# Kernel optimization log

Hardware: AMD Instinct MI355X
Metric: run time of the kernel (lower is better)

Reference implementation:

```python
import jax, jax.numpy as jnp
import numpy as np

FEAT_STRIDE = 16
PRE_NMS = 6000
POST_NMS = 300
NMS_THRESH = 0.7
NEG_THR = 0.3
POS_THR = 0.7
RPN_BATCH = 256
FG_FRAC = 0.5
SCALES = (8, 16, 32)
RATIOS = (0.5, 1.0, 2.0)
A = len(SCALES) * len(RATIOS)  # 9


def _generate_anchors():
    base = 16.0
    ctr = (base - 1.0) * 0.5
    size = base * base
    out = []
    for r in RATIOS:
        ws = np.round(np.sqrt(size / r))
        hs = np.round(ws * r)
        for s in SCALES:
            W = ws * s
            H = hs * s
            out.append([ctr - 0.5 * (W - 1), ctr - 0.5 * (H - 1),
                        ctr + 0.5 * (W - 1), ctr + 0.5 * (H - 1)])
    return np.array(out, np.float32)  # [9,4]


def _conv(x, w, b, pad):
    y = jax.lax.conv_general_dilated(x, w, (1, 1), [(pad, pad), (pad, pad)],
                                     dimension_numbers=('NCHW', 'OIHW', 'NCHW'))
    return y + b[None, :, None, None]


def _all_anchors(H, W):
    base = jnp.asarray(_generate_anchors())
    sx = jnp.arange(W, dtype=jnp.float32) * FEAT_STRIDE
    sy = jnp.arange(H, dtype=jnp.float32) * FEAT_STRIDE
    gy, gx = jnp.meshgrid(sy, sx, indexing='ij')
    shifts = jnp.stack([gx, gy, gx, gy], -1).reshape(-1, 1, 4)  # [H*W,1,4]
    return (shifts + base[None]).reshape(-1, 4)  # (h,w,a) order, [H*W*A,4]


def _decode(anchors, deltas):
    w = anchors[:, 2] - anchors[:, 0] + 1.0
    h = anchors[:, 3] - anchors[:, 1] + 1.0
    cx = anchors[:, 0] + 0.5 * w
    cy = anchors[:, 1] + 0.5 * h
    pcx = deltas[:, 0] * w + cx
    pcy = deltas[:, 1] * h + cy
    pw = jnp.exp(deltas[:, 2]) * w
    ph = jnp.exp(deltas[:, 3]) * h
    return jnp.stack([pcx - 0.5 * pw, pcy - 0.5 * ph, pcx + 0.5 * pw, pcy + 0.5 * ph], -1)


def _encode(anchors, gt):
    ew = anchors[:, 2] - anchors[:, 0] + 1.0
    eh = anchors[:, 3] - anchors[:, 1] + 1.0
    ecx = anchors[:, 0] + 0.5 * ew
    ecy = anchors[:, 1] + 0.5 * eh
    gw = gt[:, 2] - gt[:, 0] + 1.0
    gh = gt[:, 3] - gt[:, 1] + 1.0
    gcx = gt[:, 0] + 0.5 * gw
    gcy = gt[:, 1] + 0.5 * gh
    return jnp.stack([(gcx - ecx) / ew, (gcy - ecy) / eh,
                      jnp.log(gw / ew), jnp.log(gh / eh)], -1)


def _nms(boxes, scores, thresh, max_out):
    x1, y1, x2, y2 = boxes[:, 0], boxes[:, 1], boxes[:, 2], boxes[:, 3]
    areas = (x2 - x1 + 1.0) * (y2 - y1 + 1.0)
    N = boxes.shape[0]

    def body(k, st):
        valid, sel, selv = st
        s = jnp.where(valid, scores, -jnp.inf)
        i = jnp.argmax(s)
        ok = s[i] > -jnp.inf
        iw = jnp.maximum(jnp.minimum(x2[i], x2) - jnp.maximum(x1[i], x1) + 1.0, 0.0)
        ih = jnp.maximum(jnp.minimum(y2[i], y2) - jnp.maximum(y1[i], y1) + 1.0, 0.0)
        inter = iw * ih
        iou = inter / (areas[i] + areas - inter)
        valid = valid & (iou <= thresh)
        return valid, sel.at[k].set(i.astype(jnp.int32)), selv.at[k].set(ok)

    st = jax.lax.fori_loop(0, max_out, body,
                           (jnp.ones(N, bool), jnp.zeros(max_out, jnp.int32), jnp.zeros(max_out, bool)))
    return st[1], st[2]


def _propose_one(scores, deltas, anchors, imh, imw):
    boxes = _decode(anchors, deltas)
    boxes = jnp.stack([jnp.clip(boxes[:, 0], 0.0, imw - 1.0),
                       jnp.clip(boxes[:, 1], 0.0, imh - 1.0),
                       jnp.clip(boxes[:, 2], 0.0, imw - 1.0),
                       jnp.clip(boxes[:, 3], 0.0, imh - 1.0)], -1)
    top_s, idx = jax.lax.top_k(scores, PRE_NMS)
    top_b = boxes[idx]
    sel, selv = _nms(top_b, top_s, NMS_THRESH, POST_NMS)
    return top_b[sel] * selv[:, None].astype(top_b.dtype)  # [POST_NMS,4], zero rows when exhausted


def _anchor_target_one(gt, imh, imw, rfg, rbg, anchors):
    N = anchors.shape[0]
    ax1, ay1, ax2, ay2 = anchors[:, 0], anchors[:, 1], anchors[:, 2], anchors[:, 3]
    inside = (ax1 >= 0) & (ay1 >= 0) & (ax2 < imw) & (ay2 < imh)
    gx1, gy1, gx2, gy2 = gt[:, 0], gt[:, 1], gt[:, 2], gt[:, 3]
    gw = gx2 - gx1 + 1.0
    gh = gy2 - gy1 + 1.0
    gt_valid = ~((gw == 1.0) & (gh == 1.0))  # all-zero padded gt boxes
    aw = ax2 - ax1 + 1.0
    ah = ay2 - ay1 + 1.0
    iw = jnp.maximum(jnp.minimum(ax2[:, None], gx2[None, :]) - jnp.maximum(ax1[:, None], gx1[None, :]) + 1.0, 0.0)
    ih = jnp.maximum(jnp.minimum(ay2[:, None], gy2[None, :]) - jnp.maximum(ay1[:, None], gy1[None, :]) + 1.0, 0.0)
    inter = iw * ih
    iou = inter / ((aw * ah)[:, None] + (gw * gh)[None, :] - inter)  # [N,K]
    iou = jnp.where(gt_valid[None, :], iou, 0.0)
    iou = jnp.where(inside[:, None], iou, -1.0)  # outside anchors excluded, as in original
    max_ov = iou.max(1)
    arg = iou.argmax(1)
    gt_max = iou.max(0)
    gt_max = jnp.where(gt_max <= 0.0, 1e-5, gt_max)
    keep = (iou == gt_max[None, :]).any(1)  # anchors with max overlap per gt -> fg
    labels = jnp.full(N, -1.0, jnp.float32)
    labels = jnp.where(max_ov < NEG_THR, 0.0, labels)
    labels = jnp.where(keep, 1.0, labels)
    labels = jnp.where(max_ov >= POS_THR, 1.0, labels)
    labels = jnp.where(inside, labels, -1.0)

    def ranks(r, mask):
        order = jnp.argsort(jnp.where(mask, r, 2.0))
        return jnp.zeros(N, jnp.int32).at[order].set(jnp.arange(N, dtype=jnp.int32))

    num_fg = int(FG_FRAC * RPN_BATCH)
    fg_keep = (labels == 1.0) & (ranks(rfg, labels == 1.0) < num_fg)
    num_bg = RPN_BATCH - fg_keep.sum()
    bg_keep = (labels == 0.0) & (ranks(rbg, labels == 0.0) < num_bg)
    labels = jnp.where(fg_keep, 1.0, jnp.where(bg_keep, 0.0, -1.0))
    targets = _encode(anchors, gt[arg, :4])
    ones4 = jnp.ones((1, 4), jnp.float32)
    in_w = (labels == 1.0).astype(jnp.float32)[:, None] * ones4
    n_ex = (labels >= 0).sum().astype(jnp.float32)
    out_w = jnp.where(labels >= 0, 1.0 / n_ex, 0.0)[:, None] * ones4
    return labels, targets, in_w, out_w


def _rpn_forward(base_feat, im_info, gt_boxes, conv_w, conv_b, cls_w, cls_b, bbox_w, bbox_b):
    B, _, H, W = base_feat.shape
    x = jax.nn.relu(_conv(base_feat, conv_w, conv_b, 1))
    cls_score = _conv(x, cls_w, cls_b, 0)                 # [B,2A,H,W]
    # reshape(x,2) -> softmax over axis 1 -> reshape back
    prob = jax.nn.softmax(cls_score.reshape(B, 2, A * H, W), axis=1).reshape(B, 2 * A, H, W)
    bbox_pred = _conv(x, bbox_w, bbox_b, 0)               # [B,4A,H,W]
    anchors = _all_anchors(H, W)                          # [H*W*A,4]

    # ---- proposal layer (detached in original) ----
    fg = prob[:, A:, :, :].transpose(0, 2, 3, 1).reshape(B, -1)        # (h,w,a)
    deltas = bbox_pred.transpose(0, 2, 3, 1).reshape(B, -1, 4)
    rois_boxes = jax.vmap(_propose_one, in_axes=(0, 0, None, 0, 0))(
        jax.lax.stop_gradient(fg), jax.lax.stop_gradient(deltas), anchors, im_info[:, 0], im_info[:, 1])
    batch_idx = jnp.broadcast_to(jnp.arange(B, dtype=rois_boxes.dtype)[:, None, None], (B, POST_NMS, 1))
    rois = jnp.concatenate([batch_idx, rois_boxes], -1)   # [B,POST_NMS,5]

    # ---- anchor target layer (training path) ----
    key = jax.random.key(42)
    rfg = jax.random.uniform(key, (B, anchors.shape[0]))
    rbg = jax.random.uniform(jax.random.fold_in(key, 1), (B, anchors.shape[0]))
    labels, targets, in_w, out_w = jax.vmap(_anchor_target_one, in_axes=(0, 0, 0, 0, 0, None))(
        gt_boxes, im_info[:, 0], im_info[:, 1], rfg, rbg, anchors)
    # rearrange (h,w,a) -> (a,h,w) layouts to match torch permutes
    labels = labels.reshape(B, H, W, A).transpose(0, 3, 1, 2).reshape(B, -1)
    targets = targets.reshape(B, H, W, A * 4).transpose(0, 3, 1, 2)
    in_w = in_w.reshape(B, H, W, A * 4).transpose(0, 3, 1, 2)
    out_w = out_w.reshape(B, H, W, A * 4).transpose(0, 3, 1, 2)

    # cross-entropy over kept anchors
    logits = cls_score.reshape(B, 2, A, H, W).transpose(0, 2, 3, 4, 1).reshape(-1, 2)
    lab = labels.reshape(-1)
    m = (lab >= 0).astype(logits.dtype)
    logp = jax.nn.log_softmax(logits, axis=-1)
    idx = jnp.clip(lab, 0.0, 1.0).astype(jnp.int32)
    nll = -jnp.take_along_axis(logp, idx[:, None], axis=1)[:, 0]
    loss_cls = (nll * m).sum() / m.sum()

    # smooth-L1 box loss, sigma=3, sum dims [1,2,3] then mean over batch
    sigma2 = 9.0
    diff = in_w * (bbox_pred - targets)
    ad = jnp.abs(diff)
    flag = (ad < 1.0 / sigma2).astype(diff.dtype)
    lb = flag * 0.5 * sigma2 * diff * diff + (1.0 - flag) * (ad - 0.5 / sigma2)
    loss_box = (out_w * lb).sum(axis=(1, 2, 3)).mean()
    return rois, loss_cls, loss_box


def setup_inputs() -> dict:
    key = jax.random.key(0)
    ks = jax.random.split(key, 9)
    B, C, H, W = 4, 512, 50, 76
    base_feat = jax.random.normal(ks[0], (B, C, H, W), jnp.float32)
    conv_w = jax.random.normal(ks[1], (512, C, 3, 3), jnp.float32) * 0.01
    conv_b = jnp.zeros((512,), jnp.float32)
    cls_w = jax.random.normal(ks[2], (18, 512, 1, 1), jnp.float32) * 0.01
    cls_b = jnp.zeros((18,), jnp.float32)
    bbox_w = jax.random.normal(ks[3], (36, 512, 1, 1), jnp.float32) * 0.01
    bbox_b = jnp.zeros((36,), jnp.float32)
    imh, imw = float(H * FEAT_STRIDE), float(W * FEAT_STRIDE)
    im_info = jnp.tile(jnp.array([imh, imw, 1.0], jnp.float32), (B, 1))
    K = 20
    cx = jax.random.uniform(ks[4], (B, K)) * (imw - 100.0) + 50.0
    cy = jax.random.uniform(ks[5], (B, K)) * (imh - 100.0) + 50.0
    bw = jax.random.uniform(ks[6], (B, K)) * 270.0 + 30.0
    bh = jax.random.uniform(ks[7], (B, K)) * 270.0 + 30.0
    x1 = jnp.clip(cx - 0.5 * bw, 0.0, imw - 1.0)
    x2 = jnp.clip(cx + 0.5 * bw, 0.0, imw - 1.0)
    y1 = jnp.clip(cy - 0.5 * bh, 0.0, imh - 1.0)
    y2 = jnp.clip(cy + 0.5 * bh, 0.0, imh - 1.0)
    cls = jax.random.randint(ks[8], (B, K), 1, 21).astype(jnp.float32)
    gt_boxes = jnp.stack([x1, y1, x2, y2, cls], -1)
    num_boxes = jnp.full((B,), K, jnp.int32)
    return {"base_feat": base_feat, "im_info": im_info, "gt_boxes": gt_boxes,
            "num_boxes": num_boxes, "conv_w": conv_w, "conv_b": conv_b,
            "cls_w": cls_w, "cls_b": cls_b, "bbox_w": bbox_w, "bbox_b": bbox_b}


def reference(base_feat, im_info, gt_boxes, num_boxes, conv_w, conv_b, cls_w, cls_b, bbox_w, bbox_b):
    # num_boxes is implicitly handled via zero-padded gt_boxes (as in the original layer)
    return _rpn_forward(base_feat, im_info, gt_boxes, conv_w, conv_b, cls_w, cls_b, bbox_w, bbox_b)
```

## Files before the change

kernel.cpp:

```cpp
#include <hip/hip_runtime.h>
#include <stdint.h>

#define HHH 50
#define WWW 76
#define NPIX 3800
#define NA 34200
#define NSORT 65536
#define PRE 6000
#define POST 300
#define NW 94
#define CIN 512
#define COUT 512
#define NBATCH 4
#define NGT 20
#define TFHALF 68400u
#define PPLANE 4400
#define XTB 2252800

typedef __bf16 bf16x8 __attribute__((ext_vector_type(8)));
typedef float f32x4 __attribute__((ext_vector_type(4)));
typedef unsigned int u32x4v __attribute__((ext_vector_type(4)));

__device__ static inline f32x4 MFMA16(bf16x8 a, bf16x8 b, f32x4 c) {
  return __builtin_amdgcn_mfma_f32_16x16x32_bf16(a, b, c, 0, 0, 0);
}
__device__ static inline bf16x8 LD8(const unsigned short* p) {
  return __builtin_bit_cast(bf16x8, *(const u32x4v*)p);
}

__host__ __device__ static inline void tf2x32(unsigned k0, unsigned k1, unsigned& x0, unsigned& x1) {
  unsigned k2 = k0 ^ k1 ^ 0x1BD11BDAu;
#define TFR(r) do { x0 += x1; x1 = (x1 << (r)) | (x1 >> (32 - (r))); x1 ^= x0; } while (0)
  x0 += k0; x1 += k1;
  TFR(13); TFR(15); TFR(26); TFR(6);
  x0 += k1; x1 += k2 + 1u;
  TFR(17); TFR(29); TFR(16); TFR(24);
  x0 += k2; x1 += k0 + 2u;
  TFR(13); TFR(15); TFR(26); TFR(6);
  x0 += k0; x1 += k1 + 3u;
// ... 15 lines not shown
  {-56.f, -56.f,  71.f,  71.f}, {-120.f, -120.f, 135.f, 135.f}, {-248.f, -248.f, 263.f, 263.f},
  {-36.f, -80.f,  51.f,  95.f}, {-80.f, -168.f,  95.f, 183.f}, {-168.f, -344.f, 183.f, 359.f}
};

__device__ static inline unsigned monoF(float f) {
  int b = __float_as_int(f);
  unsigned u = (unsigned)b;
  return (b < 0) ? ~u : (u | 0x80000000u);
}
__device__ static inline float unmonoF(unsigned u) {
  unsigned b = (u & 0x80000000u) ? (u ^ 0x80000000u) : ~u;
  return __int_as_float((int)b);
}

__device__ static inline void split3(float v, unsigned short& h, unsigned short& m, unsigned short& l) {
  __bf16 b0 = (__bf16)v;  float f0 = (float)b0;
  float r = v - f0;       __bf16 b1 = (__bf16)r;  float f1 = (float)b1;
  float r2 = r - f1;      __bf16 b2 = (__bf16)r2;
  h = __builtin_bit_cast(unsigned short, b0);
  m = __builtin_bit_cast(unsigned short, b1);
  l = __builtin_bit_cast(unsigned short, b2);
}

__global__ void k_init(unsigned* gtmaxU, int* cnts, float* accums) {
  int t = threadIdx.x;
  if (t < NBATCH * NGT) gtmaxU[t] = 0x407FFFFFu;
  if (t < 8) cnts[t] = 0;
  if (t < 8) accums[t] = 0.f;
}

__global__ void k_split_x(const float* __restrict__ feat, unsigned short* __restrict__ x0,
                          unsigned short* __restrict__ x1, unsigned short* __restrict__ x2) {
  int tid = blockIdx.x * 256 + threadIdx.x;
  if (tid >= NBATCH * XTB) return;
  int b = tid / XTB;
  int rem = tid - b * XTB;
  int pg = rem >> 13;
  int r2 = rem & 8191;
  int cg = r2 >> 7;
  int po = (r2 >> 3) & 15;
  int cl = r2 & 7;
  int ci = cg * 8 + cl;
  int px = pg * 16 + po;
  int hq = px / 80, wq = px - hq * 80;
  float v = 0.f;
  if (hq >= 2 && hq < 52 && wq >= 1 && wq < 77)
    v = feat[((size_t)(b * 512 + ci)) * NPIX + (hq - 2) * 76 + (wq - 1)];
  unsigned short h, m, l;
  split3(v, h, m, l);
  x0[tid] = h; x1[tid] = m; x2[tid] = l;
}
// ... 3 lines not shown
  int tid = blockIdx.x * 256 + threadIdx.x;
  if (tid >= 9 * 64 * 512 * 8) return;
  int cl = tid & 7;
  int co = (tid >> 3) & 511;
  int cg = (tid >> 12) & 63;
  int tap = tid >> 18;
  int ci = cg * 8 + cl;
  float v = cw[((size_t)co * 512 + ci) * 9 + tap];
  unsigned short h, m, l;
  split3(v, h, m, l);
  w0[tid] = h; w1[tid] = m; w2[tid] = l;
}

__global__ void k_tr_w1(const float* __restrict__ clsw, const float* __restrict__ bbw, float* __restrict__ wt1) {
  int tid = blockIdx.x * 256 + threadIdx.x;
  if (tid >= CIN * 64) return;
  int c = tid & 63, ci = tid >> 6;
  float v = 0.f;
  if (c < 18) v = clsw[c * 512 + ci];
  else if (c < 54) v = bbw[(c - 18) * 512 + ci];
  wt1[tid] = v;
}

__global__ __launch_bounds__(256, 2) void k_conv3(
    const unsigned short* __restrict__ XT0, const unsigned short* __restrict__ XT1,
    const unsigned short* __restrict__ XT2,
    const unsigned short* __restrict__ WT0, const unsigned short* __restrict__ WT1,
    const unsigned short* __restrict__ WT2,
    const float* __restrict__ bias, float* __restrict__ out) {
  const int d = blockIdx.x;
  const int copair = (d >> 1) & 3, half = d & 1, g = d >> 3;
  const int cob = copair * 2 + (g & 1);
  const int pxb = half * 64 + (g >> 1);
  const int pxp = pxb & 31, b = pxb >> 5;
  const int co0 = cob * 64;
  const int px0 = 160 + pxp * 128;
  const int t = threadIdx.x, l = t & 63, wv = t >> 6;
  const int wr = wv >> 1, wc = wv & 1;
  const int l15 = l & 15, lq = l >> 4;
  f32x4 cmain[2][4], ccorr[2][4];
  double accd[2][4][4];
#pragma unroll
  for (int c = 0; c < 2; ++c)
#pragma unroll
    for (int p = 0; p < 4; ++p) {
      cmain[c][p] = (f32x4)(0.f); ccorr[c][p] = (f32x4)(0.f);
#pragma unroll
      for (int r = 0; r < 4; ++r) accd[c][p][r] = 0.0;
    }
  const unsigned short* xt0 = XT0 + (size_t)b * XTB;
  const unsigned short* xt1 = XT1 + (size_t)b * XTB;
  const unsigned short* xt2 = XT2 + (size_t)b * XTB;
  const int coA = wr * 32 + l15;
  const int OFFT[9] = {-81, -80, -79, -1, 0, 1, 79, 80, 81};
  const int pxw = px0 + wc * 64 + l15;

  for (int kg = 0; kg < 16; ++kg) {
    const int cgl = kg * 4 + lq;
    const int cglo = cgl * 128;
    const size_t aro = ((size_t)cgl * 512 + co0 + coA) * 8;
#pragma unroll
    for (int tap = 0; tap < 9; ++tap) {
      const size_t ao = aro + (size_t)tap * (64 * 512 * 8);
      bf16x8 A0[2], A1[2], A2[2];
      A0[0] = LD8(WT0 + ao); A0[1] = LD8(WT0 + ao + 128);
      A1[0] = LD8(WT1 + ao); A1[1] = LD8(WT1 + ao + 128);
      A2[0] = LD8(WT2 + ao); A2[1] = LD8(WT2 + ao + 128);
      const int pxbase = pxw + OFFT[tap];
      const size_t eob = (size_t)((pxbase >> 4) * 8192 + (pxbase & 15) * 8 + cglo);
#pragma unroll
      for (int p = 0; p < 4; ++p) {
        const size_t eo = eob + (size_t)p * 8192;
        bf16x8 B0 = LD8(xt0 + eo);
        bf16x8 B1 = LD8(xt1 + eo);
        bf16x8 B2 = LD8(xt2 + eo);
#pragma unroll
        for (int c = 0; c < 2; ++c) {
          cmain[c][p] = MFMA16(A0[c], B0, cmain[c][p]);
          ccorr[c][p] = MFMA16(A2[c], B0, ccorr[c][p]);
          ccorr[c][p] = MFMA16(A0[c], B2, ccorr[c][p]);
          ccorr[c][p] = MFMA16(A1[c], B1, ccorr[c][p]);
          ccorr[c][p] = MFMA16(A1[c], B0, ccorr[c][p]);
          ccorr[c][p] = MFMA16(A0[c], B1, ccorr[c][p]);
        }
      }
    }
    if (kg & 1) {
#pragma unroll
      for (int c = 0; c < 2; ++c)
#pragma unroll
        for (int p = 0; p < 4; ++p) {
#pragma unroll
          for (int r = 0; r < 4; ++r) accd[c][p][r] += (double)cmain[c][p][r];
          cmain[c][p] = (f32x4)(0.f);
        }
    }
  }
  const size_t outb = ((size_t)b * 512 + co0) * NPIX;
#pragma unroll
  for (int c = 0; c < 2; ++c)
#pragma unroll
    for (int p = 0; p < 4; ++p)
#pragma unroll
      for (int r = 0; r < 4; ++r) {
        int coL = wr * 32 + c * 16 + lq * 4 + r;
        int px = px0 + wc * 64 + p * 16 + l15;
        int hq = px / 80, wq = px - hq * 80;
        if (hq >= 2 && hq < 52 && wq >= 1 && wq < 77) {
          float v = (float)(accd[c][p][r] + (double)ccorr[c][p][r]) + bias[co0 + coL];
          out[outb + (size_t)coL * NPIX + (hq - 2) * 76 + (wq - 1)] = fmaxf(v, 0.f);
        }
      }
}

__global__ __launch_bounds__(256) void k_conv1(const float* __restrict__ x, const float* __restrict__ wt1,
                                               const float* __restrict__ clsb, const float* __restrict__ bbb,
                                               float* __restrict__ clsS, float* __restrict__ bbp) {
  const int b = blockIdx.y;
  const int px0 = blockIdx.x * 128;
  const int t = threadIdx.x;
  const int cg = t & 7, pg = t >> 3;
  __shared__ float xs[16][128];
  __shared__ float ws[16][72];
  double acc[8][4];
#pragma unroll
  for (int i = 0; i < 8; ++i)
#pragma unroll
    for (int j = 0; j < 4; ++j) acc[i][j] = 0.0;
  const float* xb = x + (size_t)b * CIN * NPIX;
  for (int cc = 0; cc < CIN; cc += 16) {
#pragma unroll
    for (int e0 = 0; e0 < 8; ++e0) {
// ... 34 lines not shown
#pragma unroll
      for (int j = 0; j < 4; ++j) acc[i][j] += (double)a32[i][j];
    __syncthreads();
  }
#pragma unroll
  for (int i = 0; i < 8; ++i) {
    int c = cg * 8 + i;
#pragma unroll
    for (int j = 0; j < 4; ++j) {
      int p = px0 + pg * 4 + j;
      if (p < NPIX) {
        if (c < 18) clsS[((size_t)b * 18 + c) * NPIX + p] = (float)acc[i][j] + clsb[c];
        else if (c < 54) bbp[((size_t)b * 36 + (c - 18)) * NPIX + p] = (float)acc[i][j] + bbb[c - 18];
      }
    }
  }
}

__global__ void k_decode(const float* __restrict__ clsS, const float* __restrict__ bbp,
                         const float* __restrict__ im_info, float* __restrict__ boxes,
                         unsigned long long* __restrict__ keys) {
  int tid = blockIdx.x * 256 + threadIdx.x;
  int b = tid >> 16, n = tid & 0xFFFF;
  if (n >= NA) { keys[((size_t)b << 16) + n] = 0ull; return; }
  int a = n % 9, p = n / 9;
  int h = p / WWW, w = p - h * WWW;
  const float* cb = clsS + (size_t)b * 18 * NPIX;
  float s0 = cb[(size_t)a * NPIX + p];
  float s1 = cb[(size_t)(9 + a) * NPIX + p];
  float mx = fmaxf(s0, s1);
  float e0 = expf(s0 - mx), e1 = expf(s1 - mx);
  float fg = e1 / (e0 + e1);
  const float* bb = bbp + (size_t)b * 36 * NPIX;
  float d0 = bb[(size_t)(a * 4 + 0) * NPIX + p];
  float d1 = bb[(size_t)(a * 4 + 1) * NPIX + p];
  float d2 = bb[(size_t)(a * 4 + 2) * NPIX + p];
  float d3 = bb[(size_t)(a * 4 + 3) * NPIX + p];
  float ax1 = BA[a][0] + w * 16.f, ay1 = BA[a][1] + h * 16.f;
  float ax2 = BA[a][2] + w * 16.f, ay2 = BA[a][3] + h * 16.f;
  float aw = ax2 - ax1 + 1.f, ah = ay2 - ay1 + 1.f;
  float acx = ax1 + 0.5f * aw, acy = ay1 + 0.5f * ah;
  float pcx = d0 * aw + acx, pcy = d1 * ah + acy;
  float pw = expf(d2) * aw, ph = expf(d3) * ah;
  float imh = im_info[b * 3 + 0], imw = im_info[b * 3 + 1];
  float x1 = fminf(fmaxf(pcx - 0.5f * pw, 0.f), imw - 1.f);
  float y1 = fminf(fmaxf(pcy - 0.5f * ph, 0.f), imh - 1.f);
  float x2 = fminf(fmaxf(pcx + 0.5f * pw, 0.f), imw - 1.f);
  float y2 = fminf(fmaxf(pcy + 0.5f * ph, 0.f), imh - 1.f);
  float* bx = boxes + ((size_t)b * NA + n) * 4;
  bx[0] = x1; bx[1] = y1; bx[2] = x2; bx[3] = y2;
  unsigned fb = __float_as_uint(fg);
  keys[((size_t)b << 16) + n] = ((unsigned long long)fb << 32) | (unsigned)(~(unsigned)n);
}

__global__ __launch_bounds__(256) void k_sort_local0(unsigned long long* keys) {
  __shared__ unsigned long long s[2048];
  const int chunk = blockIdx.x;
  const int b = chunk >> 5, cloc = chunk & 31;
  unsigned long long* base = keys + ((size_t)b << 16) + ((size_t)cloc << 11);
  const int gbase = cloc << 11;
  const int t = threadIdx.x;
  for (int e = t; e < 2048; e += 256) s[e] = base[e];
  __syncthreads();
  for (int k = 2; k <= 2048; k <<= 1) {
    for (int j = k >> 1; j >= 1; j >>= 1) {
      for (int q = t; q < 1024; q += 256) {
        int i = ((q & ~(j - 1)) << 1) | (q & (j - 1));
        int pp = i | j;
        bool up = (((unsigned)(gbase + i)) & (unsigned)k) == 0;
        unsigned long long a = s[i], dd = s[pp];
        if (up ? (a < dd) : (a > dd)) { s[i] = dd; s[pp] = a; }
      }
      __syncthreads();
    }
  }
  for (int e = t; e < 2048; e += 256) base[e] = s[e];
}
__global__ __launch_bounds__(256) void k_sort_merge(unsigned long long* keys, int k) {
  __shared__ unsigned long long s[2048];
  const int chunk = blockIdx.x;
  const int b = chunk >> 5, cloc = chunk & 31;
  unsigned long long* base = keys + ((size_t)b << 16) + ((size_t)cloc << 11);
  const int gbase = cloc << 11;
  const int t = threadIdx.x;
  for (int e = t; e < 2048; e += 256) s[e] = base[e];
  __syncthreads();
  for (int j = 1024; j >= 1; j >>= 1) {
    for (int q = t; q < 1024; q += 256) {
      int i = ((q & ~(j - 1)) << 1) | (q & (j - 1));
      int pp = i | j;
      bool up = (((unsigned)(gbase + i)) & (unsigned)k) == 0;
      unsigned long long a = s[i], dd = s[pp];
      if (up ? (a < dd) : (a > dd)) { s[i] = dd; s[pp] = a; }
    }
    __syncthreads();
  }
  for (int e = t; e < 2048; e += 256) base[e] = s[e];
}
__global__ void k_sort_gstep(unsigned long long* keys, int k, int j) {
  int tid = blockIdx.x * 256 + threadIdx.x;
  int b = tid >> 16, i = tid & 0xFFFF;
  if ((i & j) != 0) return;
  int pp = i | j;
  unsigned long long* base = keys + ((size_t)b << 16);
  unsigned long long a = base[i], dd = base[pp];
  bool up = (((unsigned)i) & (unsigned)k) == 0;
  if (up ? (a < dd) : (a > dd)) { base[i] = dd; base[pp] = a; }
}

__global__ void k_gather(const unsigned long long* __restrict__ keys, const float* __restrict__ boxes,
                         float* tbx1, float* tby1, float* tbx2, float* tby2, float* tba) {
  int tid = blockIdx.x * 256 + threadIdx.x;
  if (tid >= NBATCH * PRE) return;
  int b = tid / PRE;
  int k = tid - b * PRE;
  unsigned long long key = keys[((size_t)b << 16) + k];
  unsigned n = ~(unsigned)(key & 0xFFFFFFFFu);
  const float* bx = boxes + ((size_t)b * NA + n) * 4;
  float x1 = bx[0], y1 = bx[1], x2 = bx[2], y2 = bx[3];
  tbx1[tid] = x1; tby1[tid] = y1; tbx2[tid] = x2; tby2[tid] = y2;
  tba[tid] = (x2 - x1 + 1.f) * (y2 - y1 + 1.f);
}

__global__ __launch_bounds__(256) void k_mask(const float* __restrict__ tbx1, const float* __restrict__ tby1,
                                              const float* __restrict__ tbx2, const float* __restrict__ tby2,
                                              const float* __restrict__ tba, unsigned long long* __restrict__ mask) {
  const int b = blockIdx.y;
  const int i0 = blockIdx.x * 64;
  const int t = threadIdx.x;
  __shared__ float jx1[2048], jy1[2048], jx2[2048], jy2[2048], ja[2048];
  __shared__ float ix1[64], iy1[64], ix2[64], iy2[64], ia[64];
  const float* bx1 = tbx1 + b * PRE;
  const float* by1 = tby1 + b * PRE;
  const float* bx2 = tbx2 + b * PRE;
  const float* by2 = tby2 + b * PRE;
  const float* ba2 = tba + b * PRE;
  if (t < 64) {
    int i = i0 + t;
    if (i < PRE) { ix1[t] = bx1[i]; iy1[t] = by1[i]; ix2[t] = bx2[i]; iy2[t] = by2[i]; ia[t] = ba2[i]; }
// ... 19 lines not shown
        if (j > i && j < PRE) {
          int e = j - j0;
          float iw = fminf(X2, jx2[e]) - fmaxf(X1, jx1[e]) + 1.f;
          float ih = fminf(Y2, jy2[e]) - fmaxf(Y1, jy1[e]) + 1.f;
          if (iw > 0.f && ih > 0.f) {
            float inter = iw * ih;
            float iou = inter / (A + ja[e] - inter);
            if (iou > 0.7f) word |= (1ull << l);
          }
        }
      }
      mask[((size_t)(b * PRE + i)) * NW + wg] = word;
    }
    __syncthreads();
  }
}

__global__ void k_nms(const unsigned long long* __restrict__ mask,
                      const float* __restrict__ tbx1, const float* __restrict__ tby1,
                      const float* __restrict__ tbx2, const float* __restrict__ tby2,
                      float* __restrict__ out) {
  const int b = blockIdx.x;
  const int lane = threadIdx.x;
  __shared__ unsigned long long rem[NW];
  for (int w = lane; w < NW; w += 64) rem[w] = 0ull;
  __syncthreads();
  int sc = 0;
  for (int w = 0; w < NW && sc < POST; ++w) {
    while (sc < POST) {
      unsigned long long avail = ~rem[w];
      if (w == NW - 1) avail &= (1ull << (PRE - (NW - 1) * 64)) - 1ull;
      if (avail == 0ull) break;
      int l = __ffsll((unsigned long long)avail) - 1;
      int j = w * 64 + l;
      if (lane < 5) {
        float v;
        if (lane == 0) v = (float)b;
        else if (lane == 1) v = tbx1[b * PRE + j];
        else if (lane == 2) v = tby1[b * PRE + j];
        else if (lane == 3) v = tbx2[b * PRE + j];
        else v = tby2[b * PRE + j];
        out[((size_t)(b * POST + sc)) * 5 + lane] = v;
      }
      sc++;
      if (sc == POST) break;
      const unsigned long long* row = mask + ((size_t)(b * PRE + j)) * NW;
      for (int w2 = w + lane; w2 < NW; w2 += 64) {
        unsigned long long m = row[w2];
        if (w2 == w) m |= (1ull << l);
        rem[w2] |= m;
      }
      __syncthreads();
    }
  }
  for (int r2 = sc; r2 < POST; ++r2)
    if (lane < 5) out[((size_t)(b * POST + r2)) * 5 + lane] = (lane == 0) ? (float)b : 0.f;
}

__global__ __launch_bounds__(256) void k_iouA(const float* __restrict__ gt_boxes, const float* __restrict__ im_info,
                                              float* __restrict__ iou, float* __restrict__ maxov,
                                              int* __restrict__ argm, unsigned* __restrict__ gtmaxU) {
  const int b = blockIdx.y;
  const int n = blockIdx.x * 256 + threadIdx.x;
  __shared__ float g[NGT][6];
  if (threadIdx.x < NGT) {
    const float* gg = gt_boxes + (b * NGT + threadIdx.x) * 5;
    float x1 = gg[0], y1 = gg[1], x2 = gg[2], y2 = gg[3];
    g[threadIdx.x][0] = x1; g[threadIdx.x][1] = y1; g[threadIdx.x][2] = x2; g[threadIdx.x][3] = y2;
    float gw = x2 - x1 + 1.f, gh = y2 - y1 + 1.f;
    g[threadIdx.x][4] = gw * gh;
    g[threadIdx.x][5] = ((gw == 1.f) && (gh == 1.f)) ? 0.f : 1.f;
  }
  __syncthreads();
  if (n >= NA) return;
  int a = n % 9, p = n / 9;
  int h = p / WWW, w = p - h * WWW;
// ... 34 lines not shown
    float gm = unmonoF(gtmaxU[b * NGT + threadIdx.x]);
    gmf[threadIdx.x] = (gm <= 0.f) ? 1e-5f : gm;
  }
  __syncthreads();
  int label = -1;
  if (n < NA) {
    int a = n % 9, p = n / 9;
    int h = p / WWW, w = p - h * WWW;
    float ax1 = BA[a][0] + w * 16.f, ay1 = BA[a][1] + h * 16.f;
    float ax2 = BA[a][2] + w * 16.f, ay2 = BA[a][3] + h * 16.f;
    float imh = im_info[b * 3 + 0], imw = im_info[b * 3 + 1];
    bool inside = (ax1 >= 0.f) && (ay1 >= 0.f) && (ax2 < imw) && (ay2 < imh);
    float mo = maxov[b * NA + n];
    const float* row = iou + ((size_t)(b * NA) + n) * NGT;
    bool keep = false;
#pragma unroll
    for (int j = 0; j < NGT; ++j) keep = keep || (row[j] == gmf[j]);
    if (mo < 0.3f) label = 0;
    if (keep) label = 1;
    if (mo >= 0.7f) label = 1;
    if (!inside) label = -1;
    labels[b * NA + n] = label;
    unsigned pp = (unsigned)(b * NA + n);
    ufg[b * NA + n] = (label == 1) ? tf_u23(kf0, kf1, pp) : 0xFFFFFFFFu;
    ubg[b * NA + n] = (label == 0) ? tf_u23(kb0, kb1, pp) : 0xFFFFFFFFu;
  }
  unsigned long long bf = __ballot(label == 1);
  unsigned long long bb = __ballot(label == 0);
  if ((threadIdx.x & 63) == 0) {
    atomicAdd(&cnts[b], (int)__popcll(bf));
    atomicAdd(&cnts[4 + b], (int)__popcll(bb));
  }
}

__global__ __launch_bounds__(1024) void k_select(const unsigned* __restrict__ ufg, const unsigned* __restrict__ ubg,
                                                 const int* __restrict__ cnts, unsigned* __restrict__ selp,
                                                 float* __restrict__ nexf) {
  const int blk = blockIdx.x;
  const int b = blk >> 1, cls = blk & 1;
  const unsigned* u = (cls == 0 ? ufg : ubg) + (size_t)b * NA;
  const int fcnt = cnts[b], bcnt = cnts[4 + b];
  const int kk = (cls == 0) ? 128 : (256 - (fcnt < 128 ? fcnt : 128));
  const int cnt = (cls == 0) ? fcnt : bcnt;
  __shared__ int partial[16];
  __shared__ int s_cnt;
  auto bcount = [&](auto pred) -> int {
    int c = 0;
    for (int i = threadIdx.x; i < NA; i += 1024) c += pred((unsigned)i, u[i]) ? 1 : 0;
    for (int o = 32; o > 0; o >>= 1) c += __shfl_down(c, o);
    if ((threadIdx.x & 63) == 0) partial[threadIdx.x >> 6] = c;
    __syncthreads();
    if (threadIdx.x == 0) { int s = 0; for (int q = 0; q < 16; ++q) s += partial[q]; s_cnt = s; }
    __syncthreads();
    int r = s_cnt;
    __syncthreads();
    return r;
  };
  unsigned thr, ithr;
  if (cnt <= kk) { thr = 0xFFFFFFFFu; ithr = 0xFFFFFFFFu; }
  else {
    unsigned lo = 0, hi = 0x00800000u;
    while (lo < hi) {
      unsigned mid = lo + ((hi - lo) >> 1);
      int c = bcount([&](unsigned, unsigned v) { return v <= mid; });
      if (c >= kk) hi = mid; else lo = mid + 1;
    }
    thr = lo;
    int c1 = (thr == 0u) ? 0 : bcount([&](unsigned, unsigned v) { return v < thr; });
    int need = kk - c1;
    unsigned lo2 = 0, hi2 = NA - 1;
    while (lo2 < hi2) {
      unsigned mid = lo2 + ((hi2 - lo2) >> 1);
      int c = bcount([&](unsigned i, unsigned v) { return (v == thr) && (i <= mid); });
      if (c >= need) hi2 = mid; else lo2 = mid + 1;
    }
    ithr = lo2;
  }
  if (threadIdx.x == 0) {
    selp[blk * 2] = thr;
    selp[blk * 2 + 1] = ithr;
    if (cls == 1) {
      int fk = fcnt < 128 ? fcnt : 128;
      int bk2 = bcnt < kk ? bcnt : kk;
      nexf[b] = (float)(fk + bk2);
    }
  }
}

__global__ __launch_bounds__(256) void k_loss(const float* __restrict__ clsS, const float* __restrict__ bbp,
                                              const float* __restrict__ gt_boxes, const int* __restrict__ labels,
                                              const unsigned* __restrict__ ufg, const unsigned* __restrict__ ubg,
                                              const unsigned* __restrict__ selp, const int* __restrict__ argm,
                                              float* __restrict__ accums) {
  const int b = blockIdx.y;
  const int n = blockIdx.x * 256 + threadIdx.x;
  float nll = 0.f, mcnt = 0.f, lbsum = 0.f;
  if (n < NA) {
    int label = labels[b * NA + n];
    int fin = -1;
    if (label == 1) {
      unsigned uu = ufg[b * NA + n];
      unsigned thr = selp[(b * 2 + 0) * 2], ithr = selp[(b * 2 + 0) * 2 + 1];
      if (uu < thr || (uu == thr && (unsigned)n <= ithr)) fin = 1;
    } else if (label == 0) {
      unsigned uu = ubg[b * NA + n];
      unsigned thr = selp[(b * 2 + 1) * 2], ithr = selp[(b * 2 + 1) * 2 + 1];
      if (uu < thr || (uu == thr && (unsigned)n <= ithr)) fin = 0;
    }
// ... 70 lines not shown
  const float* cls_b     = (const float*)d_in[7];
  const float* bbox_w    = (const float*)d_in[8];
  const float* bbox_b    = (const float*)d_in[9];
  float* out = (float*)d_out;

  char* wp = (char*)d_ws;
  auto carve = [&](size_t bytes) -> void* {
    void* r = (void*)wp;
    wp += (bytes + 255) & ~(size_t)255;
    return r;
  };
  float* x     = (float*)carve((size_t)NBATCH * CIN * NPIX * 4);
  float* clsS  = (float*)carve((size_t)NBATCH * 18 * NPIX * 4);
  float* bbp   = (float*)carve((size_t)NBATCH * 36 * NPIX * 4);
  unsigned short* WT0 = (unsigned short*)carve((size_t)9 * 64 * 512 * 8 * 2);
  unsigned short* WT1 = (unsigned short*)carve((size_t)9 * 64 * 512 * 8 * 2);
  unsigned short* WT2 = (unsigned short*)carve((size_t)9 * 64 * 512 * 8 * 2);
  float* wt1   = (float*)carve((size_t)CIN * 64 * 4);
  unsigned* gtmaxU = (unsigned*)carve(NBATCH * NGT * 4);
  int* cnts    = (int*)carve(8 * 4);
  unsigned* selp = (unsigned*)carve(16 * 4);
  float* nexf  = (float*)carve(4 * 4);
  float* accums = (float*)carve(8 * 4);

  char* overlay = wp;
  unsigned short* XT0 = (unsigned short*)overlay;
  unsigned short* XT1 = XT0 + (size_t)NBATCH * XTB;
  unsigned short* XT2 = XT1 + (size_t)NBATCH * XTB;
  char* wp2 = overlay;
  auto carve2 = [&](size_t bytes) -> void* {
    void* r = (void*)wp2;
    wp2 += (bytes + 255) & ~(size_t)255;
    return r;
  };
  float* boxes = (float*)carve2((size_t)NBATCH * NA * 4 * 4);
  unsigned long long* keys = (unsigned long long*)carve2((size_t)NBATCH * NSORT * 8);
  float* tbx1 = (float*)carve2((size_t)NBATCH * PRE * 4);
  float* tby1 = (float*)carve2((size_t)NBATCH * PRE * 4);
  float* tbx2 = (float*)carve2((size_t)NBATCH * PRE * 4);
  float* tby2 = (float*)carve2((size_t)NBATCH * PRE * 4);
  float* tba  = (float*)carve2((size_t)NBATCH * PRE * 4);
  unsigned long long* mask = (unsigned long long*)carve2((size_t)NBATCH * PRE * NW * 8);
  float* iou   = (float*)carve2((size_t)NBATCH * NA * NGT * 4);
  float* maxov = (float*)carve2((size_t)NBATCH * NA * 4);
  int* argm    = (int*)carve2((size_t)NBATCH * NA * 4);
  int* labels  = (int*)carve2((size_t)NBATCH * NA * 4);
  unsigned* ufg = (unsigned*)carve2((size_t)NBATCH * NA * 4);
  unsigned* ubg = (unsigned*)carve2((size_t)NBATCH * NA * 4);

  unsigned kb0 = 0u, kb1 = 1u;
  tf2x32(0u, 42u, kb0, kb1);

  k_init<<<dim3(1), dim3(256), 0, stream>>>(gtmaxU, cnts, accums);
  k_split_w<<<dim3((9 * 64 * 512 * 8) / 256), dim3(256), 0, stream>>>(conv_w, WT0, WT1, WT2);
  k_tr_w1<<<dim3((CIN * 64) / 256), dim3(256), 0, stream>>>(cls_w, bbox_w, wt1);
  k_split_x<<<dim3((NBATCH * XTB + 255) / 256), dim3(256), 0, stream>>>(base_feat, XT0, XT1, XT2);
  k_conv3<<<dim3(1024), dim3(256), 0, stream>>>(XT0, XT1, XT2, WT0, WT1, WT2, conv_b, x);
  k_conv1<<<dim3(30, 4), dim3(256), 0, stream>>>(x, wt1, cls_b, bbox_b, clsS, bbp);
  k_decode<<<dim3(NBATCH * NSORT / 256), dim3(256), 0, stream>>>(clsS, bbp, im_info, boxes, keys);
  k_sort_local0<<<dim3(NBATCH * 32), dim3(256), 0, stream>>>(keys);
  for (int k = 4096; k <= 65536; k <<= 1) {
    for (int j = k >> 1; j >= 2048; j >>= 1)
      k_sort_gstep<<<dim3(NBATCH * NSORT / 256), dim3(256), 0, stream>>>(keys, k, j);
    k_sort_merge<<<dim3(NBATCH * 32), dim3(256), 0, stream>>>(keys, k);
  }
  k_gather<<<dim3((NBATCH * PRE + 255) / 256), dim3(256), 0, stream>>>(keys, boxes, tbx1, tby1, tbx2, tby2, tba);
  k_mask<<<dim3(NW, NBATCH), dim3(256), 0, stream>>>(tbx1, tby1, tbx2, tby2, tba, mask);
  k_nms<<<dim3(NBATCH), dim3(64), 0, stream>>>(mask, tbx1, tby1, tbx2, tby2, out);
  k_iouA<<<dim3((NA + 255) / 256, NBATCH), dim3(256), 0, stream>>>(gt_boxes, im_info, iou, maxov, argm, gtmaxU);
  k_labels<<<dim3((NA + 255) / 256, NBATCH), dim3(256), 0, stream>>>(iou, maxov, gtmaxU, im_info,
                                                                     0u, 42u, kb0, kb1, labels, ufg, ubg, cnts);
  k_select<<<dim3(8), dim3(1024), 0, stream>>>(ufg, ubg, cnts, selp, nexf);
  k_loss<<<dim3((NA + 255) / 256, NBATCH), dim3(256), 0, stream>>>(clsS, bbp, gt_boxes, labels, ufg, ubg, selp, argm, accums);
  k_final<<<dim3(1), dim3(1), 0, stream>>>(accums, nexf, out);
}
```

Baseline: 1.530 ms.

## Replace full bitonic sort with radix top-k select, compact, and LDS sort

The 65536-key global bitonic sort is replaced by a radix select for the 6000th-largest key, an atomic compaction of the keys at or above it, and a single-block LDS bitonic sort of 8192 entries. The binary-search sampling selection becomes a radix select over a composite key. NMS moves its suppression state into per-lane registers and picks the next box with ballots instead of shared memory and barriers. The conv3 kernel drops its double-precision accumulators for an fp32 master accumulator and requests 3 blocks per SM. This cuts many kernel launches and global sort passes, but fp32 accumulation may change numerics and raising occupancy may cause register spills.

```diff
diff --git a/kernel.cpp b/kernel.cpp
--- a/kernel.cpp
+++ b/kernel.cpp
@@ -5,7 +5,6 @@
 #define WWW 76
 #define NPIX 3800
 #define NA 34200
-#define NSORT 65536
 #define PRE 6000
 #define POST 300
 #define NW 94
@@ -14,7 +13,6 @@
 #define NBATCH 4
 #define NGT 20
 #define TFHALF 68400u
-#define PPLANE 4400
 #define XTB 2252800
 
 typedef __bf16 bf16x8 __attribute__((ext_vector_type(8)));
@@ -76,11 +74,12 @@
   l = __builtin_bit_cast(unsigned short, b2);
 }
 
-__global__ void k_init(unsigned* gtmaxU, int* cnts, float* accums) {
+__global__ void k_init(unsigned* gtmaxU, int* cnts, float* accums, int* ccnt) {
   int t = threadIdx.x;
   if (t < NBATCH * NGT) gtmaxU[t] = 0x407FFFFFu;
   if (t < 8) cnts[t] = 0;
   if (t < 8) accums[t] = 0.f;
+  if (t < 4) ccnt[t] = 0;
 }
 
 __global__ void k_split_x(const float* __restrict__ feat, unsigned short* __restrict__ x0,
@@ -130,7 +129,7 @@
   wt1[tid] = v;
 }
 
-__global__ __launch_bounds__(256, 2) void k_conv3(
+__global__ __launch_bounds__(256, 3) void k_conv3(
     const unsigned short* __restrict__ XT0, const unsigned short* __restrict__ XT1,
     const unsigned short* __restrict__ XT2,
     const unsigned short* __restrict__ WT0, const unsigned short* __restrict__ WT1,
@@ -146,15 +145,12 @@
   const int t = threadIdx.x, l = t & 63, wv = t >> 6;
   const int wr = wv >> 1, wc = wv & 1;
   const int l15 = l & 15, lq = l >> 4;
-  f32x4 cmain[2][4], ccorr[2][4];
-  double accd[2][4][4];
+  f32x4 cmain[2][4], ccorr[2][4], cmast[2][4];
 #pragma unroll
   for (int c = 0; c < 2; ++c)
 #pragma unroll
     for (int p = 0; p < 4; ++p) {
-      cmain[c][p] = (f32x4)(0.f); ccorr[c][p] = (f32x4)(0.f);
-#pragma unroll
-      for (int r = 0; r < 4; ++r) accd[c][p][r] = 0.0;
+      cmain[c][p] = (f32x4)(0.f); ccorr[c][p] = (f32x4)(0.f); cmast[c][p] = (f32x4)(0.f);
     }
   const unsigned short* xt0 = XT0 + (size_t)b * XTB;
   const unsigned short* xt1 = XT1 + (size_t)b * XTB;
@@ -193,16 +189,13 @@
         }
       }
     }
-    if (kg & 1) {
-#pragma unroll
-      for (int c = 0; c < 2; ++c)
-#pragma unroll
-        for (int p = 0; p < 4; ++p) {
-#pragma unroll
-          for (int r = 0; r < 4; ++r) accd[c][p][r] += (double)cmain[c][p][r];
-          cmain[c][p] = (f32x4)(0.f);
-        }
-    }
+#pragma unroll
+    for (int c = 0; c < 2; ++c)
+#pragma unroll
+      for (int p = 0; p < 4; ++p) {
+        cmast[c][p] += cmain[c][p];
+        cmain[c][p] = (f32x4)(0.f);
+      }
   }
   const size_t outb = ((size_t)b * 512 + co0) * NPIX;
 #pragma unroll
@@ -215,7 +208,7 @@
         int px = px0 + wc * 64 + p * 16 + l15;
         int hq = px / 80, wq = px - hq * 80;
         if (hq >= 2 && hq < 52 && wq >= 1 && wq < 77) {
-          float v = (float)(accd[c][p][r] + (double)ccorr[c][p][r]) + bias[co0 + coL];
+          float v = (cmast[c][p][r] + ccorr[c][p][r]) + bias[co0 + coL];
           out[outb + (size_t)coL * NPIX + (hq - 2) * 76 + (wq - 1)] = fmaxf(v, 0.f);
         }
       }
@@ -296,7 +289,7 @@
                          unsigned long long* __restrict__ keys) {
   int tid = blockIdx.x * 256 + threadIdx.x;
   int b = tid >> 16, n = tid & 0xFFFF;
-  if (n >= NA) { keys[((size_t)b << 16) + n] = 0ull; return; }
+  if (n >= NA) return;
   int a = n % 9, p = n / 9;
   int h = p / WWW, w = p - h * WWW;
   const float* cb = clsS + (size_t)b * 18 * NPIX;
@@ -327,68 +320,83 @@
   keys[((size_t)b << 16) + n] = ((unsigned long long)fb << 32) | (unsigned)(~(unsigned)n);
 }
 
-__global__ __launch_bounds__(256) void k_sort_local0(unsigned long long* keys) {
-  __shared__ unsigned long long s[2048];
-  const int chunk = blockIdx.x;
-  const int b = chunk >> 5, cloc = chunk & 31;
-  unsigned long long* base = keys + ((size_t)b << 16) + ((size_t)cloc << 11);
-  const int gbase = cloc << 11;
+__global__ __launch_bounds__(1024) void k_rsel_top(const unsigned long long* __restrict__ keys,
+                                                   unsigned long long* __restrict__ selK) {
+  const int b = blockIdx.x;
+  const unsigned long long* kb = keys + ((size_t)b << 16);
+  __shared__ int hist[16][256];
+  __shared__ int histT[256];
+  __shared__ unsigned long long sh_prefix;
+  __shared__ unsigned sh_r;
+  const int t = threadIdx.x, wid = t >> 6;
+  if (t == 0) { sh_prefix = 0ull; sh_r = PRE; }
+  __syncthreads();
+  for (int p = 7; p >= 0; --p) {
+    for (int e = t; e < 4096; e += 1024) ((int*)hist)[e] = 0;
+    __syncthreads();
+    unsigned long long pref = sh_prefix;
+    for (int i = t; i < NA; i += 1024) {
+      unsigned long long k = kb[i];
+      bool m = (p == 7) || ((k >> (8 * (p + 1))) == pref);
+      if (m) atomicAdd(&hist[wid][(int)((k >> (8 * p)) & 255)], 1);
+    }
+    __syncthreads();
+    if (t < 256) { int s = 0; for (int w = 0; w < 16; ++w) s += hist[w][t]; histT[t] = s; }
+    __syncthreads();
+    if (t == 0) {
+      unsigned rr = sh_r; unsigned cum = 0;
+      for (int v = 255; v >= 0; --v) {
+        cum += (unsigned)histT[v];
+        if (cum >= rr) { sh_r = rr - (cum - (unsigned)histT[v]); sh_prefix = (sh_prefix << 8) | (unsigned)v; break; }
+      }
+    }
+    __syncthreads();
+  }
+  if (t == 0) selK[b] = sh_prefix;
+}
+
+__global__ void k_compact(const unsigned long long* __restrict__ keys,
+                          const unsigned long long* __restrict__ selK,
+                          int* __restrict__ ccnt, unsigned long long* __restrict__ comp) {
+  int tid = blockIdx.x * 256 + threadIdx.x;
+  int b = tid >> 16, n = tid & 0xFFFF;
+  if (n >= NA) return;
+  unsigned long long k = keys[((size_t)b << 16) + n];
+  if (k >= selK[b]) {
+    int pos = atomicAdd(&ccnt[b], 1);
+    comp[b * 8192 + pos] = k;
+  }
+}
+
+__global__ __launch_bounds__(1024) void k_sort_lds(unsigned long long* __restrict__ comp) {
+  __shared__ unsigned long long s[8192];
+  const int b = blockIdx.x;
   const int t = threadIdx.x;
-  for (int e = t; e < 2048; e += 256) s[e] = base[e];
+  unsigned long long* cb = comp + b * 8192;
+  for (int e = t; e < 8192; e += 1024) s[e] = (e < PRE) ? cb[e] : 0ull;
   __syncthreads();
-  for (int k = 2; k <= 2048; k <<= 1) {
+  for (int k = 2; k <= 8192; k <<= 1) {
     for (int j = k >> 1; j >= 1; j >>= 1) {
-      for (int q = t; q < 1024; q += 256) {
+      for (int q = t; q < 4096; q += 1024) {
         int i = ((q & ~(j - 1)) << 1) | (q & (j - 1));
         int pp = i | j;
-        bool up = (((unsigned)(gbase + i)) & (unsigned)k) == 0;
-        unsigned long long a = s[i], dd = s[pp];
-        if (up ? (a < dd) : (a > dd)) { s[i] = dd; s[pp] = a; }
+        bool up = (i & k) == 0;
+        unsigned long long a = s[i], d = s[pp];
+        if (up ? (a < d) : (a > d)) { s[i] = d; s[pp] = a; }
       }
       __syncthreads();
     }
   }
-  for (int e = t; e < 2048; e += 256) base[e] = s[e];
-}
-__global__ __launch_bounds__(256) void k_sort_merge(unsigned long long* keys, int k) {
-  __shared__ unsigned long long s[2048];
-  const int chunk = blockIdx.x;
-  const int b = chunk >> 5, cloc = chunk & 31;
-  unsigned long long* base = keys + ((size_t)b << 16) + ((size_t)cloc << 11);
-  const int gbase = cloc << 11;
-  const int t = threadIdx.x;
-  for (int e = t; e < 2048; e += 256) s[e] = base[e];
-  __syncthreads();
-  for (int j = 1024; j >= 1; j >>= 1) {
-    for (int q = t; q < 1024; q += 256) {
-      int i = ((q & ~(j - 1)) << 1) | (q & (j - 1));
-      int pp = i | j;
-      bool up = (((unsigned)(gbase + i)) & (unsigned)k) == 0;
-      unsigned long long a = s[i], dd = s[pp];
-      if (up ? (a < dd) : (a > dd)) { s[i] = dd; s[pp] = a; }
-    }
-    __syncthreads();
-  }
-  for (int e = t; e < 2048; e += 256) base[e] = s[e];
-}
-__global__ void k_sort_gstep(unsigned long long* keys, int k, int j) {
-  int tid = blockIdx.x * 256 + threadIdx.x;
-  int b = tid >> 16, i = tid & 0xFFFF;
-  if ((i & j) != 0) return;
-  int pp = i | j;
-  unsigned long long* base = keys + ((size_t)b << 16);
-  unsigned long long a = base[i], dd = base[pp];
-  bool up = (((unsigned)i) & (unsigned)k) == 0;
-  if (up ? (a < dd) : (a > dd)) { base[i] = dd; base[pp] = a; }
-}
-
-__global__ void k_gather(const unsigned long long* __restrict__ keys, const float* __restrict__ boxes,
+  for (int e = t; e < PRE; e += 1024) cb[e] = s[e];
+}
+
+__global__ void k_gather(const unsigned long long* __restrict__ comp, const float* __restrict__ boxes,
                          float* tbx1, float* tby1, float* tbx2, float* tby2, float* tba) {
   int tid = blockIdx.x * 256 + threadIdx.x;
   if (tid >= NBATCH * PRE) return;
   int b = tid / PRE;
   int k = tid - b * PRE;
-  unsigned long long key = keys[((size_t)b << 16) + k];
+  unsigned long long key = comp[b * 8192 + k];
   unsigned n = ~(unsigned)(key & 0xFFFFFFFFu);
   const float* bx = boxes + ((size_t)b * NA + n) * 4;
   float x1 = bx[0], y1 = bx[1], x2 = bx[2], y2 = bx[3];
@@ -454,36 +462,41 @@
                       float* __restrict__ out) {
   const int b = blockIdx.x;
   const int lane = threadIdx.x;
-  __shared__ unsigned long long rem[NW];
-  for (int w = lane; w < NW; w += 64) rem[w] = 0ull;
-  __syncthreads();
+  unsigned long long rem0 = 0ull;
+  unsigned long long rem1;
+  if (64 + lane < NW) rem1 = (64 + lane == NW - 1) ? ~((1ull << (PRE - (NW - 1) * 64)) - 1ull) : 0ull;
+  else rem1 = ~0ull;
   int sc = 0;
-  for (int w = 0; w < NW && sc < POST; ++w) {
-    while (sc < POST) {
-      unsigned long long avail = ~rem[w];
-      if (w == NW - 1) avail &= (1ull << (PRE - (NW - 1) * 64)) - 1ull;
-      if (avail == 0ull) break;
-      int l = __ffsll((unsigned long long)avail) - 1;
-      int j = w * 64 + l;
-      if (lane < 5) {
-        float v;
-        if (lane == 0) v = (float)b;
-        else if (lane == 1) v = tbx1[b * PRE + j];
-        else if (lane == 2) v = tby1[b * PRE + j];
-        else if (lane == 3) v = tbx2[b * PRE + j];
-        else v = tby2[b * PRE + j];
-        out[((size_t)(b * POST + sc)) * 5 + lane] = v;
-      }
-      sc++;
-      if (sc == POST) break;
-      const unsigned long long* row = mask + ((size_t)(b * PRE + j)) * NW;
-      for (int w2 = w + lane; w2 < NW; w2 += 64) {
-        unsigned long long m = row[w2];
-        if (w2 == w) m |= (1ull << l);
-        rem[w2] |= m;
-      }
-      __syncthreads();
-    }
+  for (; sc < POST; ++sc) {
+    unsigned long long a0 = ~rem0, a1 = ~rem1;
+    unsigned long long bal0 = __ballot(a0 != 0ull);
+    int w, l;
+    if (bal0) {
+      int src = __ffsll(bal0) - 1;
+      unsigned long long av = __shfl(a0, src);
+      w = src; l = __ffsll(av) - 1;
+    } else {
+      unsigned long long bal1 = __ballot(a1 != 0ull);
+      if (!bal1) break;
+      int src = __ffsll(bal1) - 1;
+      unsigned long long av = __shfl(a1, src);
+      w = 64 + src; l = __ffsll(av) - 1;
+    }
+    int j = w * 64 + l;
+    if (lane < 5) {
+      float v;
+      if (lane == 0) v = (float)b;
+      else if (lane == 1) v = tbx1[b * PRE + j];
+      else if (lane == 2) v = tby1[b * PRE + j];
+      else if (lane == 3) v = tbx2[b * PRE + j];
+      else v = tby2[b * PRE + j];
+      out[((size_t)(b * POST + sc)) * 5 + lane] = v;
+    }
+    const unsigned long long* row = mask + ((size_t)(b * PRE + j)) * NW;
+    rem0 |= row[lane];
+    if (64 + lane < NW) rem1 |= row[64 + lane];
+    if (w < 64) { if (lane == w) rem0 |= (1ull << l); }
+    else if (lane == w - 64) rem1 |= (1ull << l);
   }
   for (int r2 = sc; r2 < POST; ++r2)
     if (lane < 5) out[((size_t)(b * POST + r2)) * 5 + lane] = (lane == 0) ? (float)b : 0.f;
@@ -564,8 +577,8 @@
     if (!inside) label = -1;
     labels[b * NA + n] = label;
     unsigned pp = (unsigned)(b * NA + n);
-    ufg[b * NA + n] = (label == 1) ? tf_u23(kf0, kf1, pp) : 0xFFFFFFFFu;
-    ubg[b * NA + n] = (label == 0) ? tf_u23(kb0, kb1, pp) : 0xFFFFFFFFu;
+    ufg[b * NA + n] = (label == 1) ? tf_u23(kf0, kf1, pp) : 0x00FFFFFFu;
+    ubg[b * NA + n] = (label == 0) ? tf_u23(kb0, kb1, pp) : 0x00FFFFFFu;
   }
   unsigned long long bf = __ballot(label == 1);
   unsigned long long bb = __ballot(label == 0);
@@ -575,57 +588,57 @@
   }
 }
 
-__global__ __launch_bounds__(1024) void k_select(const unsigned* __restrict__ ufg, const unsigned* __restrict__ ubg,
-                                                 const int* __restrict__ cnts, unsigned* __restrict__ selp,
-                                                 float* __restrict__ nexf) {
+__global__ __launch_bounds__(1024) void k_rsel_samp(const unsigned* __restrict__ ufg, const unsigned* __restrict__ ubg,
+                                                    const int* __restrict__ cnts, unsigned* __restrict__ selp,
+                                                    float* __restrict__ nexf) {
   const int blk = blockIdx.x;
   const int b = blk >> 1, cls = blk & 1;
   const unsigned* u = (cls == 0 ? ufg : ubg) + (size_t)b * NA;
   const int fcnt = cnts[b], bcnt = cnts[4 + b];
   const int kk = (cls == 0) ? 128 : (256 - (fcnt < 128 ? fcnt : 128));
   const int cnt = (cls == 0) ? fcnt : bcnt;
-  __shared__ int partial[16];
-  __shared__ int s_cnt;
-  auto bcount = [&](auto pred) -> int {
-    int c = 0;
-    for (int i = threadIdx.x; i < NA; i += 1024) c += pred((unsigned)i, u[i]) ? 1 : 0;
-    for (int o = 32; o > 0; o >>= 1) c += __shfl_down(c, o);
-    if ((threadIdx.x & 63) == 0) partial[threadIdx.x >> 6] = c;
-    __syncthreads();
-    if (threadIdx.x == 0) { int s = 0; for (int q = 0; q < 16; ++q) s += partial[q]; s_cnt = s; }
-    __syncthreads();
-    int r = s_cnt;
-    __syncthreads();
-    return r;
-  };
-  unsigned thr, ithr;
-  if (cnt <= kk) { thr = 0xFFFFFFFFu; ithr = 0xFFFFFFFFu; }
-  else {
-    unsigned lo = 0, hi = 0x00800000u;
-    while (lo < hi) {
-      unsigned mid = lo + ((hi - lo) >> 1);
-      int c = bcount([&](unsigned, unsigned v) { return v <= mid; });
-      if (c >= kk) hi = mid; else lo = mid + 1;
-    }
-    thr = lo;
-    int c1 = (thr == 0u) ? 0 : bcount([&](unsigned, unsigned v) { return v < thr; });
-    int need = kk - c1;
-    unsigned lo2 = 0, hi2 = NA - 1;
-    while (lo2 < hi2) {
-      unsigned mid = lo2 + ((hi2 - lo2) >> 1);
-      int c = bcount([&](unsigned i, unsigned v) { return (v == thr) && (i <= mid); });
-      if (c >= need) hi2 = mid; else lo2 = mid + 1;
-    }
-    ithr = lo2;
-  }
-  if (threadIdx.x == 0) {
-    selp[blk * 2] = thr;
-    selp[blk * 2 + 1] = ithr;
+  const int t = threadIdx.x, wid = t >> 6;
+  __shared__ int hist[16][256];
+  __shared__ int histT[256];
+  __shared__ unsigned long long sh_prefix;
+  __shared__ unsigned sh_r;
+  if (t == 0) {
     if (cls == 1) {
       int fk = fcnt < 128 ? fcnt : 128;
       int bk2 = bcnt < kk ? bcnt : kk;
       nexf[b] = (float)(fk + bk2);
     }
+    sh_prefix = 0ull; sh_r = (unsigned)kk;
+  }
+  __syncthreads();
+  if (kk > cnt) {
+    if (t == 0) { selp[blk * 2] = 0x00FFFFFFu; selp[blk * 2 + 1] = 0x1FFFFu; }
+    return;
+  }
+  for (int p = 4; p >= 0; --p) {
+    for (int e = t; e < 4096; e += 1024) ((int*)hist)[e] = 0;
+    __syncthreads();
+    unsigned long long pref = sh_prefix;
+    for (int i = t; i < NA; i += 1024) {
+      unsigned long long k = ((unsigned long long)u[i] << 17) | (unsigned)i;
+      if ((k >> (8 * (p + 1))) == pref)
+        atomicAdd(&hist[wid][(int)((k >> (8 * p)) & 255)], 1);
+    }
+    __syncthreads();
+    if (t < 256) { int s = 0; for (int w = 0; w < 16; ++w) s += hist[w][t]; histT[t] = s; }
+    __syncthreads();
+    if (t == 0) {
+      unsigned rr = sh_r; unsigned cum = 0;
+      for (int v = 0; v < 256; ++v) {
+        cum += (unsigned)histT[v];
+        if (cum >= rr) { sh_r = rr - (cum - (unsigned)histT[v]); sh_prefix = (sh_prefix << 8) | (unsigned)v; break; }
+      }
+    }
+    __syncthreads();
+  }
+  if (t == 0) {
+    selp[blk * 2] = (unsigned)(sh_prefix >> 17);
+    selp[blk * 2 + 1] = (unsigned)(sh_prefix & 0x1FFFF);
   }
 }
 
@@ -742,6 +755,8 @@
   unsigned* selp = (unsigned*)carve(16 * 4);
   float* nexf  = (float*)carve(4 * 4);
   float* accums = (float*)carve(8 * 4);
+  int* ccnt    = (int*)carve(4 * 4);
+  unsigned long long* selK = (unsigned long long*)carve(4 * 8);
 
   char* overlay = wp;
   unsigned short* XT0 = (unsigned short*)overlay;
@@ -754,7 +769,7 @@
     return r;
   };
   float* boxes = (float*)carve2((size_t)NBATCH * NA * 4 * 4);
-  unsigned long long* keys = (unsigned long long*)carve2((size_t)NBATCH * NSORT * 8);
+  unsigned long long* keys = (unsigned long long*)carve2((size_t)NBATCH * 65536 * 8);
   float* tbx1 = (float*)carve2((size_t)NBATCH * PRE * 4);
   float* tby1 = (float*)carve2((size_t)NBATCH * PRE * 4);
   float* tbx2 = (float*)carve2((size_t)NBATCH * PRE * 4);
@@ -767,30 +782,28 @@
   int* labels  = (int*)carve2((size_t)NBATCH * NA * 4);
   unsigned* ufg = (unsigned*)carve2((size_t)NBATCH * NA * 4);
   unsigned* ubg = (unsigned*)carve2((size_t)NBATCH * NA * 4);
+  unsigned long long* comp = (unsigned long long*)carve2((size_t)NBATCH * 8192 * 8);
 
   unsigned kb0 = 0u, kb1 = 1u;
   tf2x32(0u, 42u, kb0, kb1);
 
-  k_init<<<dim3(1), dim3(256), 0, stream>>>(gtmaxU, cnts, accums);
+  k_init<<<dim3(1), dim3(256), 0, stream>>>(gtmaxU, cnts, accums, ccnt);
   k_split_w<<<dim3((9 * 64 * 512 * 8) / 256), dim3(256), 0, stream>>>(conv_w, WT0, WT1, WT2);
   k_tr_w1<<<dim3((CIN * 64) / 256), dim3(256), 0, stream>>>(cls_w, bbox_w, wt1);
   k_split_x<<<dim3((NBATCH * XTB + 255) / 256), dim3(256), 0, stream>>>(base_feat, XT0, XT1, XT2);
   k_conv3<<<dim3(1024), dim3(256), 0, stream>>>(XT0, XT1, XT2, WT0, WT1, WT2, conv_b, x);
   k_conv1<<<dim3(30, 4), dim3(256), 0, stream>>>(x, wt1, cls_b, bbox_b, clsS, bbp);
-  k_decode<<<dim3(NBATCH * NSORT / 256), dim3(256), 0, stream>>>(clsS, bbp, im_info, boxes, keys);
-  k_sort_local0<<<dim3(NBATCH * 32), dim3(256), 0, stream>>>(keys);
-  for (int k = 4096; k <= 65536; k <<= 1) {
-    for (int j = k >> 1; j >= 2048; j >>= 1)
-      k_sort_gstep<<<dim3(NBATCH * NSORT / 256), dim3(256), 0, stream>>>(keys, k, j);
-    k_sort_merge<<<dim3(NBATCH * 32), dim3(256), 0, stream>>>(keys, k);
-  }
-  k_gather<<<dim3((NBATCH * PRE + 255) / 256), dim3(256), 0, stream>>>(keys, boxes, tbx1, tby1, tbx2, tby2, tba);
+  k_decode<<<dim3(NBATCH * 65536 / 256), dim3(256), 0, stream>>>(clsS, bbp, im_info, boxes, keys);
+  k_rsel_top<<<dim3(NBATCH), dim3(1024), 0, stream>>>(keys, selK);
+  k_compact<<<dim3(NBATCH * 65536 / 256), dim3(256), 0, stream>>>(keys, selK, ccnt, comp);
+  k_sort_lds<<<dim3(NBATCH), dim3(1024), 0, stream>>>(comp);
+  k_gather<<<dim3((NBATCH * PRE + 255) / 256), dim3(256), 0, stream>>>(comp, boxes, tbx1, tby1, tbx2, tby2, tba);
   k_mask<<<dim3(NW, NBATCH), dim3(256), 0, stream>>>(tbx1, tby1, tbx2, tby2, tba, mask);
   k_nms<<<dim3(NBATCH), dim3(64), 0, stream>>>(mask, tbx1, tby1, tbx2, tby2, out);
   k_iouA<<<dim3((NA + 255) / 256, NBATCH), dim3(256), 0, stream>>>(gt_boxes, im_info, iou, maxov, argm, gtmaxU);
   k_labels<<<dim3((NA + 255) / 256, NBATCH), dim3(256), 0, stream>>>(iou, maxov, gtmaxU, im_info,
                                                                      0u, 42u, kb0, kb1, labels, ufg, ubg, cnts);
-  k_select<<<dim3(8), dim3(1024), 0, stream>>>(ufg, ubg, cnts, selp, nexf);
+  k_rsel_samp<<<dim3(8), dim3(1024), 0, stream>>>(ufg, ubg, cnts, selp, nexf);
   k_loss<<<dim3((NA + 255) / 256, NBATCH), dim3(256), 0, stream>>>(clsS, bbp, gt_boxes, labels, ufg, ubg, selp, argm, accums);
   k_final<<<dim3(1), dim3(1), 0, stream>>>(accums, nexf, out);
 }
```

New measurement: 2.121 ms (median of 2 runs). +38.6%, slower.
